# Kernel tuning notes

Hardware: AMD Instinct MI355X
Metric: run time of the kernel (lower is better)

The kernel has to match this reference:

```python
import jax, jax.numpy as jnp
import numpy as np

B, NQ, NK = 16, 2048, 2048
KD, QD, KQ = 256, 256, 256
CLIP = 10.0


def setup_inputs() -> dict:
    key = jax.random.key(0)
    k1, k2, k3, k4, k5 = jax.random.split(key, 5)
    k_inputs = jax.random.normal(k1, (B, NK, KD), dtype=jnp.float32)
    q_inputs = jax.random.normal(k2, (B, NQ, QD), dtype=jnp.float32)
    adjancy = jax.random.randint(k3, (B, NQ, NK), 0, 2, dtype=jnp.int32)
    # Linear init in source: (rand - 0.5) * 0.05 -> uniform(-0.025, 0.025)
    Wk = jax.random.uniform(k4, (KD, KQ), dtype=jnp.float32, minval=-0.025, maxval=0.025)
    Wq = jax.random.uniform(k5, (QD, KQ), dtype=jnp.float32, minval=-0.025, maxval=0.025)
    return {"k_inputs": k_inputs, "q_inputs": q_inputs, "adjancy": adjancy, "Wk": Wk, "Wq": Wq}


def reference(k_inputs, q_inputs, adjancy, Wk, Wq):
    k = jnp.einsum("bnd,de->bne", k_inputs, Wk)          # [B, NK, KQ]
    q = jnp.einsum("bmd,de->bme", q_inputs, Wq)          # [B, NQ, KQ]
    scale = 1.0 / jnp.sqrt(jnp.asarray(KQ, dtype=q.dtype))
    scores = jnp.einsum("bme,bne->bmn", q, k) * scale     # [B, NQ, NK]
    scores = jnp.tanh(scores) * CLIP                      # clip is not None
    scores = jnp.where(adjancy.astype(bool), scores, -jnp.inf)
    return jax.nn.softmax(scores, axis=2)
```

## Files before the change

kernel.cpp:

```cpp
#include <hip/hip_runtime.h>

#define BATCH 16
#define NQ 2048
#define NK 2048
#define KD 256

typedef short s16x8 __attribute__((ext_vector_type(8)));
typedef __bf16 bf16x8 __attribute__((ext_vector_type(8)));
typedef float f32x16 __attribute__((ext_vector_type(16)));
typedef float f32x4 __attribute__((ext_vector_type(4)));

static __device__ __forceinline__ unsigned short f2bf(float f) {
  unsigned u = __builtin_bit_cast(unsigned, f);
  u += 0x7FFFu + ((u >> 16) & 1u);
  return (unsigned short)(u >> 16);
}

static __device__ __forceinline__ float bf2f(unsigned short h) {
  return __builtin_bit_cast(float, (unsigned)h << 16);
}

static __device__ __forceinline__ f32x16 mfma_bf16(s16x8 a, s16x8 b, f32x16 c) {
  return __builtin_amdgcn_mfma_f32_32x32x16_bf16(
      __builtin_bit_cast(bf16x8, a), __builtin_bit_cast(bf16x8, b), c, 0, 0, 0);
}

__global__ void prep_wt(const float* __restrict__ Wk, unsigned short* __restrict__ WkT,
                        const float* __restrict__ Wq, unsigned short* __restrict__ WqT) {
  const float* W = blockIdx.y ? Wq : Wk;
  unsigned short* WT = blockIdx.y ? WqT : WkT;
  float scale = blockIdx.y ? 0.0625f : 1.0f;
  int idx = blockIdx.x * 256 + threadIdx.x;
  int n = idx >> 8, k = idx & 255;
  WT[n * 256 + k] = f2bf(W[k * 256 + n] * scale);
}

__global__ __launch_bounds__(256, 2) void proj_kernel(
    const float* __restrict__ Xk, const unsigned short* __restrict__ WkT,
    unsigned short* __restrict__ Yk,
    const float* __restrict__ Xq, const unsigned short* __restrict__ WqT,
    unsigned short* __restrict__ Yq) {
  const float* X;
  const unsigned short* WT;
  unsigned short* Y;
  if (blockIdx.y == 0) { X = Xk; WT = WkT; Y = Yk; }
  else                 { X = Xq; WT = WqT; Y = Yq; }

  int tid = threadIdx.x;
  int wave = tid >> 6, lane = tid & 63;
  int l31 = lane & 31, kh = lane >> 5;
  int r0 = blockIdx.x * 128 + wave * 32;

  const float* xp = X + (size_t)(r0 + l31) * 256 + kh * 8;

  f32x16 acc[8];
#pragma unroll
  for (int ct = 0; ct < 8; ++ct)
#pragma unroll
    for (int i = 0; i < 16; ++i) acc[ct][i] = 0.0f;

#pragma unroll
  for (int kk = 0; kk < 16; ++kk) {
    f32x4 a0 = *(const f32x4*)(xp + kk * 16);
    f32x4 a1 = *(const f32x4*)(xp + kk * 16 + 4);
    s16x8 af;
#pragma unroll
    for (int j = 0; j < 4; ++j) {
      af[j]     = (short)f2bf(a0[j]);
      af[4 + j] = (short)f2bf(a1[j]);
    }
#pragma unroll
    for (int ct = 0; ct < 8; ++ct) {
      s16x8 bw = *(const s16x8*)(WT + (size_t)(ct * 32 + l31) * 256 + kk * 16 + kh * 8);
      acc[ct] = mfma_bf16(af, bw, acc[ct]);
    }
  }

  size_t gbase = (size_t)(r0 >> 5) * 16;
#pragma unroll
  for (int ct = 0; ct < 8; ++ct) {
    int ecol = ct * 32 + l31;
    size_t cbase = (gbase + (ecol >> 4)) * 64 * 8 + ((ecol >> 3) & 1) * 32 * 8 + (ecol & 7);
#pragma unroll
    for (int r = 0; r < 16; ++r) {
      int rrow = (r & 3) + 8 * (r >> 2) + 4 * kh;
      Y[cbase + rrow * 8] = f2bf(acc[ct][r]);
    }
  }
}

__global__ __launch_bounds__(512, 2) void attn_kernel(
    const unsigned short* __restrict__ Kf, const unsigned short* __restrict__ Qf,
    const int* __restrict__ adj, float* __restrict__ out) {
  int lin = blockIdx.y * 64 + blockIdx.x;
  int b  = (lin & 7) * 2 + ((lin >> 3) & 1);
  int qt = lin >> 4;
  int q0 = qt * 32;
  int tid = threadIdx.x;
  int wave = tid >> 6, lane = tid & 63;
  int l31 = lane & 31, kh = lane >> 5;
  int colbase = wave * 256;

  __shared__ unsigned lmask[32 * 64];
  __shared__ float wsum[8][32];
  __shared__ float rrecip[32];

  const int* abase = adj + ((size_t)b * NQ + q0) * (size_t)NK;
#pragma unroll
  for (int rr4 = 0; rr4 < 4; ++rr4) {
    int rr = wave * 4 + rr4;
    const int* ap = abase + (size_t)rr * NK + lane;
    int av[32];
#pragma unroll
    for (int c = 0; c < 32; ++c) av[c] = ap[c * 64];
    unsigned my = 0;
#pragma unroll
    for (int c = 0; c < 32; ++c) {
      unsigned long long m = __ballot(av[c] != 0);
      if ((lane >> 1) == c) my = (lane & 1) ? (unsigned)(m >> 32) : (unsigned)m;
    }
    lmask[rr * 64 + lane] = my;
  }

  const unsigned short* qp = Qf + ((size_t)(b * 64 + qt) * 16) * 512;
  s16x8 aq[16];
#pragma unroll
  for (int kk = 0; kk < 16; ++kk)
    aq[kk] = *(const s16x8*)(qp + (kk * 64 + lane) * 8);

  const unsigned short* kfb = Kf + ((size_t)b * 64 * 16) * 512;

  __syncthreads();

  float rsum[16];
#pragma unroll
  for (int r = 0; r < 16; ++r) rsum[r] = 0.0f;

  s16x8 pst[8][2];
  unsigned bit = 1u << l31;

#pragma unroll
  for (int ct = 0; ct < 8; ++ct) {
    f32x16 acc;
#pragma unroll
    for (int i = 0; i < 16; ++i) acc[i] = 0.0f;

    const unsigned short* kpt = kfb + ((size_t)(wave * 8 + ct) * 16) * 512;
#pragma unroll
    for (int kk = 0; kk < 16; ++kk) {
      s16x8 bk = *(const s16x8*)(kpt + (kk * 64 + lane) * 8);
      acc = mfma_bf16(aq[kk], bk, acc);
    }

#pragma unroll
    for (int r = 0; r < 16; ++r) {
      int rrow = (r & 3) + 8 * (r >> 2) + 4 * kh;
      unsigned mw = lmask[rrow * 64 + wave * 8 + ct];
      float s = acc[r];
      float u  = __builtin_amdgcn_exp2f(s * 2.885390081777927f);
      float th = 1.0f - 2.0f * __builtin_amdgcn_rcpf(u + 1.0f);
      float e  = __builtin_amdgcn_exp2f((10.0f * th - 10.0f) * 1.44269504088896f);
      float p  = (mw & bit) ? e : 0.0f;
      rsum[r] += p;
      pst[ct][r >> 3][r & 7] = (short)f2bf(p);
    }
  }

#pragma unroll
  for (int r = 0; r < 16; ++r) {
    float v = rsum[r];
    v += __shfl_xor(v, 1);
    v += __shfl_xor(v, 2);
    v += __shfl_xor(v, 4);
    v += __shfl_xor(v, 8);
    v += __shfl_xor(v, 16);
    rsum[r] = v;
  }
  if (l31 == 0) {
#pragma unroll
    for (int r = 0; r < 16; ++r)
      wsum[wave][(r & 3) + 8 * (r >> 2) + 4 * kh] = rsum[r];
  }
  __syncthreads();
  if (tid < 32) {
    float s = 0.0f;
#pragma unroll
    for (int w = 0; w < 8; ++w) s += wsum[w][tid];
    rrecip[tid] = 1.0f / s;
  }
  __syncthreads();

  float rc[16];
#pragma unroll
  for (int r = 0; r < 16; ++r) rc[r] = rrecip[(r & 3) + 8 * (r >> 2) + 4 * kh];

  float* op = out + ((size_t)b * NQ + q0) * (size_t)NK + colbase + l31;
#pragma unroll
  for (int ct = 0; ct < 8; ++ct) {
#pragma unroll
    for (int r = 0; r < 16; ++r) {
      int rrow = (r & 3) + 8 * (r >> 2) + 4 * kh;
      float pf = bf2f((unsigned short)pst[ct][r >> 3][r & 7]);
      op[(size_t)rrow * NK + ct * 32] = pf * rc[r];
    }
  }
}

extern "C" void kernel_launch(void* const* d_in, const int* in_sizes, int n_in,
                              void* d_out, int out_size, void* d_ws, size_t ws_size,
                              hipStream_t stream) {
  const float* k_in = (const float*)d_in[0];
  const float* q_in = (const float*)d_in[1];
  const int* adj    = (const int*)d_in[2];
  const float* Wk   = (const float*)d_in[3];
  const float* Wq   = (const float*)d_in[4];
  float* out = (float*)d_out;

  char* ws = (char*)d_ws;
  unsigned short* WkT = (unsigned short*)(ws);
  unsigned short* WqT = (unsigned short*)(ws + (1u << 17));
  unsigned short* Kf  = (unsigned short*)(ws + (1u << 18));
  unsigned short* Qf  = (unsigned short*)(ws + (1u << 18) + (1u << 24));

  prep_wt<<<dim3(256, 2), 256, 0, stream>>>(Wk, WkT, Wq, WqT);

  proj_kernel<<<dim3(256, 2), 256, 0, stream>>>(k_in, WkT, Kf, q_in, WqT, Qf);

  attn_kernel<<<dim3(64, 16), 512, 0, stream>>>(Kf, Qf, adj, out);
}
```

Measured before the change: 263.3 us.

## Make adjacency mask per-wave for its own column slice and drop block barrier

Each wave now loads and ballots only the adjacency columns it consumes (its 256-column slice across all 32 rows) and stores the bits in a private LDS region. This removes the __syncthreads before the QK loop and lets waves start computing independently. Q fragment loads are also issued before the mask loads so the two overlap. Correctness relies on each wave writing and reading only its own LDS slice; the loads become 32 rows by 4 columns per lane instead of 4 rows by 32 columns.

```diff
diff --git a/kernel.cpp b/kernel.cpp
--- a/kernel.cpp
+++ b/kernel.cpp
@@ -101,36 +101,43 @@
   int l31 = lane & 31, kh = lane >> 5;
   int colbase = wave * 256;
 
-  __shared__ unsigned lmask[32 * 64];
+  __shared__ unsigned lmask[8 * 256];
   __shared__ float wsum[8][32];
   __shared__ float rrecip[32];
 
-  const int* abase = adj + ((size_t)b * NQ + q0) * (size_t)NK;
-#pragma unroll
-  for (int rr4 = 0; rr4 < 4; ++rr4) {
-    int rr = wave * 4 + rr4;
-    const int* ap = abase + (size_t)rr * NK + lane;
-    int av[32];
-#pragma unroll
-    for (int c = 0; c < 32; ++c) av[c] = ap[c * 64];
-    unsigned my = 0;
-#pragma unroll
-    for (int c = 0; c < 32; ++c) {
-      unsigned long long m = __ballot(av[c] != 0);
-      if ((lane >> 1) == c) my = (lane & 1) ? (unsigned)(m >> 32) : (unsigned)m;
-    }
-    lmask[rr * 64 + lane] = my;
-  }
-
   const unsigned short* qp = Qf + ((size_t)(b * 64 + qt) * 16) * 512;
   s16x8 aq[16];
 #pragma unroll
   for (int kk = 0; kk < 16; ++kk)
     aq[kk] = *(const s16x8*)(qp + (kk * 64 + lane) * 8);
 
+  const int* abase = adj + ((size_t)b * NQ + q0) * (size_t)NK + colbase + lane;
+  unsigned* lm = lmask + wave * 256;
+#pragma unroll
+  for (int rg = 0; rg < 4; ++rg) {
+    int av[8][4];
+#pragma unroll
+    for (int r8 = 0; r8 < 8; ++r8) {
+      const int* ap = abase + (size_t)(rg * 8 + r8) * NK;
+#pragma unroll
+      for (int cc = 0; cc < 4; ++cc) av[r8][cc] = ap[cc * 64];
+    }
+#pragma unroll
+    for (int r8 = 0; r8 < 8; ++r8) {
+      unsigned long long b0 = __ballot(av[r8][0] != 0);
+      unsigned long long b1 = __ballot(av[r8][1] != 0);
+      unsigned long long b2 = __ballot(av[r8][2] != 0);
+      unsigned long long b3 = __ballot(av[r8][3] != 0);
+      if (lane < 8) {
+        unsigned long long bb = (lane & 4) ? ((lane & 2) ? b3 : b2)
+                                           : ((lane & 2) ? b1 : b0);
+        unsigned word = (lane & 1) ? (unsigned)(bb >> 32) : (unsigned)bb;
+        lm[(rg * 8 + r8) * 8 + lane] = word;
+      }
+    }
+  }
+
   const unsigned short* kfb = Kf + ((size_t)b * 64 * 16) * 512;
-
-  __syncthreads();
 
   float rsum[16];
 #pragma unroll
@@ -155,7 +162,7 @@
 #pragma unroll
     for (int r = 0; r < 16; ++r) {
       int rrow = (r & 3) + 8 * (r >> 2) + 4 * kh;
-      unsigned mw = lmask[rrow * 64 + wave * 8 + ct];
+      unsigned mw = lm[rrow * 8 + ct];
       float s = acc[r];
       float u  = __builtin_amdgcn_exp2f(s * 2.885390081777927f);
       float th = 1.0f - 2.0f * __builtin_amdgcn_rcpf(u + 1.0f);
```

Result: no change. 260.5 us (-1.1%).
